# Optimization experiments

Measured on AMD Instinct MI355X. Metric: run time of the kernel, lower is better.

## Reference

```python
import jax, jax.numpy as jnp
import numpy as np

D_MODEL = 1024
N_HEADS = 16
D_HEAD = D_MODEL // N_HEADS
D_FF = 4096
EPS = 1e-5


def layernorm(x, gamma, beta):
    mu = jnp.mean(x, axis=-1, keepdims=True)
    var = jnp.var(x, axis=-1, keepdims=True)
    return (x - mu) * jax.lax.rsqrt(var + EPS) * gamma + beta


def setup_inputs() -> dict:
    key = jax.random.key(0)
    ks = jax.random.split(key, 16)
    B, T = 4, 2048
    s = 1.0 / np.sqrt(D_MODEL)
    sf = 1.0 / np.sqrt(D_FF)
    return {
        "x": jax.random.normal(ks[0], (B, T, D_MODEL), jnp.float32),
        "gate_score": jax.random.uniform(ks[1], (B,), jnp.float32),
        "Wq": jax.random.normal(ks[2], (D_MODEL, D_MODEL), jnp.float32) * s,
        "bq": jnp.zeros((D_MODEL,), jnp.float32),
        "Wk": jax.random.normal(ks[3], (D_MODEL, D_MODEL), jnp.float32) * s,
        "bk": jnp.zeros((D_MODEL,), jnp.float32),
        "Wv": jax.random.normal(ks[4], (D_MODEL, D_MODEL), jnp.float32) * s,
        "bv": jnp.zeros((D_MODEL,), jnp.float32),
        "Wo": jax.random.normal(ks[5], (D_MODEL, D_MODEL), jnp.float32) * s,
        "bo": jnp.zeros((D_MODEL,), jnp.float32),
        "W1": jax.random.normal(ks[6], (D_MODEL, D_FF), jnp.float32) * s,
        "b1": jnp.zeros((D_FF,), jnp.float32),
        "W2": jax.random.normal(ks[7], (D_FF, D_MODEL), jnp.float32) * sf,
        "b2": jnp.zeros((D_MODEL,), jnp.float32),
        "gamma1": jnp.ones((D_MODEL,), jnp.float32),
        "beta1": jnp.zeros((D_MODEL,), jnp.float32),
        "gamma2": jnp.ones((D_MODEL,), jnp.float32),
        "beta2": jnp.zeros((D_MODEL,), jnp.float32),
    }


def reference(x, gate_score, Wq, bq, Wk, bk, Wv, bv, Wo, bo,
              W1, b1, W2, b2, gamma1, beta1, gamma2, beta2):
    B, T, C = x.shape
    # --- attention sub-block (pre-norm) ---
    h = layernorm(x, gamma1, beta1)
    Q = (h @ Wq + bq).reshape(B, T, N_HEADS, D_HEAD).transpose(0, 2, 1, 3)
    K = (h @ Wk + bk).reshape(B, T, N_HEADS, D_HEAD).transpose(0, 2, 1, 3)
    V = (h @ Wv + bv).reshape(B, T, N_HEADS, D_HEAD).transpose(0, 2, 1, 3)
    scores = jnp.einsum("bhqd,bhkd->bhqk", Q, K) / np.sqrt(D_HEAD)
    causal = jnp.tril(jnp.ones((T, T), dtype=bool))  # True = keep
    scores = jnp.where(causal, scores, -jnp.inf)
    attn = jax.nn.softmax(scores, axis=-1)
    ctx = jnp.einsum("bhqk,bhkd->bhqd", attn, V)
    ctx = ctx.transpose(0, 2, 1, 3).reshape(B, T, C)
    attn_out = ctx @ Wo + bo
    x1 = x + attn_out
    # --- FFN sub-block (pre-norm) ---
    h2 = layernorm(x1, gamma2, beta2)
    ff = jax.nn.gelu(h2 @ W1 + b1, approximate=False) @ W2 + b2
    x2 = x1 + ff
    # --- gated residual ---
    g = gate_score[:, None, None]
    return x + g * (x2 - x)
```

## Files before the change

kernel.cpp:

```cpp
#include <hip/hip_runtime.h>
#include <hip/hip_bf16.h>
#include <cmath>

typedef unsigned short u16;
typedef __attribute__((ext_vector_type(8))) short short8;
typedef __attribute__((ext_vector_type(4))) float f32x4;

#define DM 1024
#define NH 16
#define DH 64
#define DFF 4096
#define BB 4
#define TT 2048
#define MROWS (BB*TT)

__device__ __forceinline__ float bu2f(u16 u) {
    union { float f; unsigned v; } c; c.v = ((unsigned)u) << 16; return c.f;
}
__device__ __forceinline__ u16 f2bu(float f) {
    __hip_bfloat16 h = __float2bfloat16(f);
    union { __hip_bfloat16 h; u16 u; } c; c.h = h; return c.u;
}
__device__ __forceinline__ void async_copy16(const u16* g, u16* l) {
    __builtin_amdgcn_global_load_lds((const __attribute__((address_space(1))) void*)g,
                                     (__attribute__((address_space(3))) void*)l, 16, 0, 0);
}

__global__ void ln_kernel(const float* __restrict__ x, const float* __restrict__ gamma,
                          const float* __restrict__ beta, u16* __restrict__ out)
{
    int row = blockIdx.x;
    int tid = threadIdx.x;
    float4 v4 = ((const float4*)(x + (size_t)row * DM))[tid];
    float v[4] = { v4.x, v4.y, v4.z, v4.w };
    float s = v[0] + v[1] + v[2] + v[3];
    float ss = v[0]*v[0] + v[1]*v[1] + v[2]*v[2] + v[3]*v[3];
    #pragma unroll
    for (int o = 32; o > 0; o >>= 1) { s += __shfl_down(s, o); ss += __shfl_down(ss, o); }
    __shared__ float red[8];
    int w = tid >> 6;
    if ((tid & 63) == 0) { red[w] = s; red[4 + w] = ss; }
    __syncthreads();
    s  = red[0] + red[1] + red[2] + red[3];
    ss = red[4] + red[5] + red[6] + red[7];
    float mu  = s * (1.0f / DM);
    float var = ss * (1.0f / DM) - mu * mu;
    float rstd = rsqrtf(var + 1e-5f);
    float4 g4 = ((const float4*)gamma)[tid];
    float4 b4 = ((const float4*)beta)[tid];
    float g[4] = { g4.x, g4.y, g4.z, g4.w };
    float b[4] = { b4.x, b4.y, b4.z, b4.w };
    ushort4 o4;
    u16* op = (u16*)&o4;
    #pragma unroll
    for (int i = 0; i < 4; i++) op[i] = f2bu((v[i] - mu) * rstd * g[i] + b[i]);
    ((ushort4*)(out + (size_t)row * DM))[tid] = o4;
}

__global__ void transpose4_f2b(const float* __restrict__ w0, const float* __restrict__ w1,
                               const float* __restrict__ w2, const float* __restrict__ w3,
                               u16* __restrict__ outQKV, u16* __restrict__ outO)
{
    __shared__ u16 tile[32][33];
    const float* in = (blockIdx.z == 0) ? w0 : (blockIdx.z == 1) ? w1
                     : (blockIdx.z == 2) ? w2 : w3;
    u16* out = (blockIdx.z < 3) ? (outQKV + (size_t)blockIdx.z * DM * DM) : outO;
    int bx = blockIdx.x * 32;
    int by = blockIdx.y * 32;
    int tx = threadIdx.x, ty = threadIdx.y;
    #pragma unroll
    for (int i = 0; i < 32; i += 8)
        tile[ty + i][tx] = f2bu(in[(size_t)(by + ty + i) * DM + bx + tx]);
    __syncthreads();
    #pragma unroll
    for (int i = 0; i < 32; i += 8)
        out[(size_t)(bx + ty + i) * DM + by + tx] = tile[tx][ty + i];
}

__global__ void transpose_f2b(const float* __restrict__ in, u16* __restrict__ out,
                              int R, int C)
{
    __shared__ u16 tile[32][33];
    int bx = blockIdx.x * 32;
    int by = blockIdx.y * 32;
    int tx = threadIdx.x, ty = threadIdx.y;
    #pragma unroll
    for (int i = 0; i < 32; i += 8)
        tile[ty + i][tx] = f2bu(in[(size_t)(by + ty + i) * C + bx + tx]);
    __syncthreads();
    #pragma unroll
    for (int i = 0; i < 32; i += 8)
        out[(size_t)(bx + ty + i) * R + by + tx] = tile[tx][ty + i];
}

#define BM 128
#define BN 128
#define BK 32

template<int EPI>
__global__ void gemm_bt(
    const u16* __restrict__ A, const u16* __restrict__ Bt,
    const float* __restrict__ bias, const float* __restrict__ bias2,
    const float* __restrict__ bias3, void* __restrict__ Cv,
    const float* __restrict__ res, const float* __restrict__ x0,
    const float* __restrict__ gate, int M, int N, int K)
{
    __shared__ __align__(16) u16 As[BM * BK];
    __shared__ __align__(16) u16 Bs[BN * BK];
    int tid = threadIdx.x;
    int lane = tid & 63, wave = tid >> 6;
    int wm = (wave & 1) * 64, wn = (wave >> 1) * 64;
    int lm = lane & 15, quad = lane >> 4;
    size_t row0 = (size_t)blockIdx.x * BM;
    size_t col0 = (size_t)blockIdx.y * BN;

    int sr = tid >> 2;
    int sk = (tid & 3) * 8;
    const u16* Ag = A  + (row0 + sr) * (size_t)K + sk;
    const u16* Bg = Bt + (col0 + sr) * (size_t)K + sk;
    u16* Asl = As + tid * 8;
    u16* Bsl = Bs + tid * 8;

    f32x4 acc[4][4];
    #pragma unroll
    for (int i = 0; i < 4; i++)
        #pragma unroll
        for (int j = 0; j < 4; j++)
            acc[i][j] = (f32x4){0.f, 0.f, 0.f, 0.f};

    for (int k0 = 0; k0 < K; k0 += BK) {
        __syncthreads();
        async_copy16(Ag + k0,                  Asl);
        async_copy16(Ag + (size_t)64 * K + k0, Asl + 64 * BK);
        async_copy16(Bg + k0,                  Bsl);
        async_copy16(Bg + (size_t)64 * K + k0, Bsl + 64 * BK);
        __syncthreads();
        short8 af[4], bfr[4];
        #pragma unroll
        for (int t = 0; t < 4; t++) {
            af[t]  = *(const short8*)&As[(wm + t * 16 + lm) * BK + quad * 8];
            bfr[t] = *(const short8*)&Bs[(wn + t * 16 + lm) * BK + quad * 8];
        }
        #pragma unroll
        for (int mt = 0; mt < 4; mt++)
            #pragma unroll
            for (int nt = 0; nt < 4; nt++)
                acc[mt][nt] = __builtin_amdgcn_mfma_f32_16x16x32_bf16(
                    af[mt], bfr[nt], acc[mt][nt], 0, 0, 0);
    }

    u16*   C16 = (u16*)Cv;
    float* Cf  = (float*)Cv;

    const float* bb = bias;
    size_t csub = 0;
    if (EPI == 0 && bias2 != nullptr) {
        size_t cbase = col0 + wn;
        if (cbase >= 2048)      { bb = bias3; csub = 2048; }
        else if (cbase >= 1024) { bb = bias2; csub = 1024; }
    }

    #pragma unroll
    for (int mt = 0; mt < 4; mt++) {
        #pragma unroll
        for (int nt = 0; nt < 4; nt++) {
            #pragma unroll
            for (int r = 0; r < 4; r++) {
                size_t row = row0 + wm + mt * 16 + quad * 4 + r;
                size_t col = col0 + wn + nt * 16 + lm;
                size_t idx = row * (size_t)N + col;
                float v = acc[mt][nt][r] + bb[col - csub];
                if (EPI == 0) {
                    C16[idx] = f2bu(v);
                } else if (EPI == 1) {
                    Cf[idx] = v + res[idx];
                } else if (EPI == 2) {
                    v = 0.5f * v * (1.0f + erff(v * 0.70710678118f));
                    C16[idx] = f2bu(v);
                } else {
                    float xv  = x0[idx];
                    float x1v = res[idx];
                    float g   = gate[row >> 11];
                    Cf[idx] = xv + g * (x1v + v - xv);
                }
            }
        }
    }
}

#define AVS 72

__global__ __launch_bounds__(256, 4) void attn_mfma(
    const u16* __restrict__ QKV, u16* __restrict__ ctx)
{
    __shared__ __align__(16) u16 Kl[64][AVS];
    __shared__ __align__(16) u16 Vt[64][AVS];
    __shared__ __align__(16) u16 Pl[4][16][AVS];

    const int LD = 3 * DM;
    int tid = threadIdx.x, lane = tid & 63, w = tid >> 6;
    int lm = lane & 15, quad = lane >> 4;

    int bi = blockIdx.x;
    int pair = bi & 15, h = (bi >> 4) & 15, b = bi >> 8;
    int t1 = 31 - pair, t2 = pair;

    const size_t hoff = (size_t)h * DH;
    const u16* Qp = QKV + (size_t)b * TT * LD + hoff;
    const u16* Kp = Qp + DM;
    const u16* Vp = Qp + 2 * DM;

    short8 aqA[2], aqB[2];
    #pragma unroll
    for (int dc = 0; dc < 2; dc++) {
        aqA[dc] = *(const short8*)(Qp + (size_t)(t1 * 64 + w * 16 + lm) * LD + dc * 32 + quad * 8);
        aqB[dc] = *(const short8*)(Qp + (size_t)(t2 * 64 + w * 16 + lm) * LD + dc * 32 + quad * 8);
    }

    int kkey = tid & 63, kdim = (tid >> 6) * 16;
    int vkey = (tid & 31) * 2, vdim = (tid >> 5) * 8;

    const u16* kb0 = Kp + (size_t)kkey * LD + kdim;
    const u16* vb0 = Vp + (size_t)vkey * LD + vdim;
    const u16* vb1 = Vp + (size_t)(vkey + 1) * LD + vdim;

    const float sc = 0.18033688011f;
    const float FM = 24.0f;
    const short s1 = (short)0x3F80;
    const short8 ones = (short8){s1, s1, s1, s1, s1, s1, s1, s1};

    uint4 kr0 = *(const uint4*)(kb0);
    uint4 kr1 = *(const uint4*)(kb0 + 8);
    uint4 vr0 = *(const uint4*)(vb0);
    uint4 vr1 = *(const uint4*)(vb1);

    #pragma unroll
    for (int ti = 0; ti < 2; ti++) {
        int tcur = (ti == 0) ? t1 : t2;
        int nch = tcur + 1;
        int q0 = tcur * 64;
        int qw = q0 + w * 16;
        short8 a0 = (ti == 0) ? aqA[0] : aqB[0];
        short8 a1 = (ti == 0) ? aqA[1] : aqB[1];
        int qv = qw + lm;

        f32x4 o[4], o5;
        #pragma unroll
        for (int ds = 0; ds < 4; ds++) o[ds] = (f32x4){0.f, 0.f, 0.f, 0.f};
        o5 = (f32x4){0.f, 0.f, 0.f, 0.f};

        for (int c = 0; c < nch; c++) {
            int kb = c * 64;
            __syncthreads();
            *(uint4*)&Kl[kkey][kdim]     = kr0;
            *(uint4*)&Kl[kkey][kdim + 8] = kr1;
            {
                const u16* p0 = (const u16*)&vr0;
                const u16* p1 = (const u16*)&vr1;
                #pragma unroll
                for (int j = 0; j < 8; j++) {
                    ushort2 pk = { p0[j], p1[j] };
                    *(ushort2*)&Vt[vdim + j][vkey] = pk;
                }
            }
            __syncthreads();

            {
                size_t offn = (c + 1 < nch) ? (size_t)(c + 1) * 64 * LD : 0;
                kr0 = *(const uint4*)(kb0 + offn);
                kr1 = *(const uint4*)(kb0 + offn + 8);
                vr0 = *(const uint4*)(vb0 + offn);
                vr1 = *(const uint4*)(vb1 + offn);
            }

            f32x4 s[4];
            #pragma unroll
            for (int ks = 0; ks < 4; ks++) s[ks] = (f32x4){0.f, 0.f, 0.f, 0.f};
            #pragma unroll
            for (int ks = 0; ks < 4; ks++) {
                short8 k0 = *(const short8*)&Kl[ks * 16 + lm][quad * 8];
                short8 k1 = *(const short8*)&Kl[ks * 16 + lm][32 + quad * 8];
                s[ks] = __builtin_amdgcn_mfma_f32_16x16x32_bf16(k0, a0, s[ks], 0, 0, 0);
                s[ks] = __builtin_amdgcn_mfma_f32_16x16x32_bf16(k1, a1, s[ks], 0, 0, 0);
            }

            bool mz = (kb + 63 > qw);
            #pragma unroll
            for (int ks = 0; ks < 4; ks++) {
                int kbase = kb + ks * 16 + quad * 4;
                ushort4 pk;
                u16* pp = (u16*)&pk;
                #pragma unroll
                for (int r = 0; r < 4; r++) {
                    float v = s[ks][r] * sc - FM;
                    if (mz && (kbase + r > qv)) v = -INFINITY;
                    pp[r] = f2bu(exp2f(v));
                }
                *(ushort4*)&Pl[w][lm][ks * 16 + quad * 4] = pk;
            }

            #pragma unroll
            for (int kc = 0; kc < 2; kc++) {
                short8 ap = *(const short8*)&Pl[w][lm][kc * 32 + quad * 8];
                #pragma unroll
                for (int ds = 0; ds < 4; ds++) {
                    short8 bv = *(const short8*)&Vt[ds * 16 + lm][kc * 32 + quad * 8];
                    o[ds] = __builtin_amdgcn_mfma_f32_16x16x32_bf16(ap, bv, o[ds], 0, 0, 0);
                }
                o5 = __builtin_amdgcn_mfma_f32_16x16x32_bf16(ap, ones, o5, 0, 0, 0);
            }
        }

        float inv[4];
        #pragma unroll
        for (int r = 0; r < 4; r++) inv[r] = 1.0f / o5[r];
        #pragma unroll
        for (int ds = 0; ds < 4; ds++)
            #pragma unroll
            for (int r = 0; r < 4; r++) {
                size_t row = (size_t)(b * TT + qw + quad * 4 + r);
                ctx[row * DM + hoff + ds * 16 + lm] = f2bu(o[ds][r] * inv[r]);
            }
    }
}

extern "C" void kernel_launch(void* const* d_in, const int* in_sizes, int n_in,
                              void* d_out, int out_size, void* d_ws, size_t ws_size,
                              hipStream_t stream)
{
    const float* x    = (const float*)d_in[0];
    const float* gate = (const float*)d_in[1];
    const float* Wq   = (const float*)d_in[2];
    const float* bq   = (const float*)d_in[3];
    const float* Wk   = (const float*)d_in[4];
    const float* bk   = (const float*)d_in[5];
    const float* Wv   = (const float*)d_in[6];
    const float* bv   = (const float*)d_in[7];
    const float* Wo   = (const float*)d_in[8];
    const float* bo   = (const float*)d_in[9];
    const float* W1   = (const float*)d_in[10];
    const float* b1   = (const float*)d_in[11];
    const float* W2   = (const float*)d_in[12];
    const float* b2   = (const float*)d_in[13];
    const float* gamma1 = (const float*)d_in[14];
    const float* beta1  = (const float*)d_in[15];
    const float* gamma2 = (const float*)d_in[16];
    const float* beta2  = (const float*)d_in[17];
    float* out = (float*)d_out;

    char* ws = (char*)d_ws;
    const size_t MB = 1024 * 1024;
    u16* WtQKV = (u16*)(ws + 0 * MB);
    u16* WtO   = (u16*)(ws + 6 * MB);
    u16* Wt1   = (u16*)(ws + 8 * MB);
    u16* Wt2   = (u16*)(ws + 16 * MB);
    u16* h     = (u16*)(ws + 24 * MB);
    u16* ctx   = (u16*)(ws + 24 * MB);
    u16* QKVb  = (u16*)(ws + 40 * MB);
    float* x1  = (float*)(ws + 40 * MB);
    u16* h2    = (u16*)(ws + 72 * MB);
    u16* ff    = (u16*)(ws + 88 * MB);

    dim3 tb(32, 8);
    transpose4_f2b<<<dim3(32, 32, 4), tb, 0, stream>>>(Wq, Wk, Wv, Wo, WtQKV, WtO);
    transpose_f2b<<<dim3(DFF / 32, DM / 32), tb, 0, stream>>>(W1, Wt1, DM, DFF);
    transpose_f2b<<<dim3(DM / 32, DFF / 32), tb, 0, stream>>>(W2, Wt2, DFF, DM);

    ln_kernel<<<MROWS, 256, 0, stream>>>(x, gamma1, beta1, h);

    gemm_bt<0><<<dim3(MROWS / BM, 3 * DM / BN), 256, 0, stream>>>(
        h, WtQKV, bq, bk, bv, QKVb, nullptr, nullptr, nullptr, MROWS, 3 * DM, DM);

    attn_mfma<<<BB * NH * 16, 256, 0, stream>>>(QKVb, ctx);

    gemm_bt<1><<<dim3(MROWS / BM, DM / BN), 256, 0, stream>>>(
        ctx, WtO, bo, nullptr, nullptr, x1, x, nullptr, nullptr, MROWS, DM, DM);

    ln_kernel<<<MROWS, 256, 0, stream>>>(x1, gamma2, beta2, h2);

    gemm_bt<2><<<dim3(MROWS / BM, DFF / BN), 256, 0, stream>>>(
        h2, Wt1, b1, nullptr, nullptr, ff, nullptr, nullptr, nullptr, MROWS, DFF, DM);

    gemm_bt<3><<<dim3(MROWS / BM, DM / BN), 256, 0, stream>>>(
        ff, Wt2, b2, nullptr, nullptr, out, x1, x, gate, MROWS, DM, DFF);
}
```

Measured before the change: 559.5 us.

## Double GEMM K-tile with XOR-swizzled LDS and split attention blocks per query tile

```diff
diff --git a/kernel.cpp b/kernel.cpp
--- a/kernel.cpp
+++ b/kernel.cpp
@@ -95,7 +95,7 @@
 
 #define BM 128
 #define BN 128
-#define BK 32
+#define BK 64
 
 template<int EPI>
 __global__ void gemm_bt(
@@ -114,12 +114,15 @@
     size_t row0 = (size_t)blockIdx.x * BM;
     size_t col0 = (size_t)blockIdx.y * BN;
 
-    int sr = tid >> 2;
-    int sk = (tid & 3) * 8;
-    const u16* Ag = A  + (row0 + sr) * (size_t)K + sk;
-    const u16* Bg = Bt + (col0 + sr) * (size_t)K + sk;
+    int sr = tid >> 3;
+    int scol = (((tid & 7) ^ (sr & 7)) * 8);
+    const u16* Ag = A  + (row0 + sr) * (size_t)K + scol;
+    const u16* Bg = Bt + (col0 + sr) * (size_t)K + scol;
     u16* Asl = As + tid * 8;
     u16* Bsl = Bs + tid * 8;
+
+    int fc0 = ((0 * 4 + quad) ^ (lm & 7)) * 8;
+    int fc1 = ((1 * 4 + quad) ^ (lm & 7)) * 8;
 
     f32x4 acc[4][4];
     #pragma unroll
@@ -131,22 +134,30 @@
     for (int k0 = 0; k0 < K; k0 += BK) {
         __syncthreads();
         async_copy16(Ag + k0,                  Asl);
+        async_copy16(Ag + (size_t)32 * K + k0, Asl + 32 * BK);
         async_copy16(Ag + (size_t)64 * K + k0, Asl + 64 * BK);
+        async_copy16(Ag + (size_t)96 * K + k0, Asl + 96 * BK);
         async_copy16(Bg + k0,                  Bsl);
+        async_copy16(Bg + (size_t)32 * K + k0, Bsl + 32 * BK);
         async_copy16(Bg + (size_t)64 * K + k0, Bsl + 64 * BK);
+        async_copy16(Bg + (size_t)96 * K + k0, Bsl + 96 * BK);
         __syncthreads();
-        short8 af[4], bfr[4];
-        #pragma unroll
-        for (int t = 0; t < 4; t++) {
-            af[t]  = *(const short8*)&As[(wm + t * 16 + lm) * BK + quad * 8];
-            bfr[t] = *(const short8*)&Bs[(wn + t * 16 + lm) * BK + quad * 8];
-        }
-        #pragma unroll
-        for (int mt = 0; mt < 4; mt++)
-            #pragma unroll
-            for (int nt = 0; nt < 4; nt++)
-                acc[mt][nt] = __builtin_amdgcn_mfma_f32_16x16x32_bf16(
-                    af[mt], bfr[nt], acc[mt][nt], 0, 0, 0);
+        #pragma unroll
+        for (int ks = 0; ks < 2; ks++) {
+            int fc = ks ? fc1 : fc0;
+            short8 af[4], bfr[4];
+            #pragma unroll
+            for (int t = 0; t < 4; t++) {
+                af[t]  = *(const short8*)&As[(wm + t * 16 + lm) * BK + fc];
+                bfr[t] = *(const short8*)&Bs[(wn + t * 16 + lm) * BK + fc];
+            }
+            #pragma unroll
+            for (int mt = 0; mt < 4; mt++)
+                #pragma unroll
+                for (int nt = 0; nt < 4; nt++)
+                    acc[mt][nt] = __builtin_amdgcn_mfma_f32_16x16x32_bf16(
+                        af[mt], bfr[nt], acc[mt][nt], 0, 0, 0);
+        }
     }
 
     u16*   C16 = (u16*)Cv;
@@ -190,7 +201,7 @@
 
 #define AVS 72
 
-__global__ __launch_bounds__(256, 4) void attn_mfma(
+__global__ __launch_bounds__(256, 5) void attn_mfma(
     const u16* __restrict__ QKV, u16* __restrict__ ctx)
 {
     __shared__ __align__(16) u16 Kl[64][AVS];
@@ -202,20 +213,21 @@
     int lm = lane & 15, quad = lane >> 4;
 
     int bi = blockIdx.x;
-    int pair = bi & 15, h = (bi >> 4) & 15, b = bi >> 8;
-    int t1 = 31 - pair, t2 = pair;
+    int tcur = 31 - (bi & 31);
+    int h = (bi >> 5) & 15, b = bi >> 9;
 
     const size_t hoff = (size_t)h * DH;
     const u16* Qp = QKV + (size_t)b * TT * LD + hoff;
     const u16* Kp = Qp + DM;
     const u16* Vp = Qp + 2 * DM;
 
-    short8 aqA[2], aqB[2];
-    #pragma unroll
-    for (int dc = 0; dc < 2; dc++) {
-        aqA[dc] = *(const short8*)(Qp + (size_t)(t1 * 64 + w * 16 + lm) * LD + dc * 32 + quad * 8);
-        aqB[dc] = *(const short8*)(Qp + (size_t)(t2 * 64 + w * 16 + lm) * LD + dc * 32 + quad * 8);
-    }
+    int nch = tcur + 1;
+    int q0 = tcur * 64;
+    int qw = q0 + w * 16;
+    int qv = qw + lm;
+
+    short8 a0 = *(const short8*)(Qp + (size_t)(qw + lm) * LD + quad * 8);
+    short8 a1 = *(const short8*)(Qp + (size_t)(qw + lm) * LD + 32 + quad * 8);
 
     int kkey = tid & 63, kdim = (tid >> 6) * 16;
     int vkey = (tid & 31) * 2, vdim = (tid >> 5) * 8;
@@ -234,94 +246,83 @@
     uint4 vr0 = *(const uint4*)(vb0);
     uint4 vr1 = *(const uint4*)(vb1);
 
-    #pragma unroll
-    for (int ti = 0; ti < 2; ti++) {
-        int tcur = (ti == 0) ? t1 : t2;
-        int nch = tcur + 1;
-        int q0 = tcur * 64;
-        int qw = q0 + w * 16;
-        short8 a0 = (ti == 0) ? aqA[0] : aqB[0];
-        short8 a1 = (ti == 0) ? aqA[1] : aqB[1];
-        int qv = qw + lm;
-
-        f32x4 o[4], o5;
-        #pragma unroll
-        for (int ds = 0; ds < 4; ds++) o[ds] = (f32x4){0.f, 0.f, 0.f, 0.f};
-        o5 = (f32x4){0.f, 0.f, 0.f, 0.f};
-
-        for (int c = 0; c < nch; c++) {
-            int kb = c * 64;
-            __syncthreads();
-            *(uint4*)&Kl[kkey][kdim]     = kr0;
-            *(uint4*)&Kl[kkey][kdim + 8] = kr1;
-            {
-                const u16* p0 = (const u16*)&vr0;
-                const u16* p1 = (const u16*)&vr1;
-                #pragma unroll
-                for (int j = 0; j < 8; j++) {
-                    ushort2 pk = { p0[j], p1[j] };
-                    *(ushort2*)&Vt[vdim + j][vkey] = pk;
-                }
-            }
-            __syncthreads();
-
-            {
-                size_t offn = (c + 1 < nch) ? (size_t)(c + 1) * 64 * LD : 0;
-                kr0 = *(const uint4*)(kb0 + offn);
-                kr1 = *(const uint4*)(kb0 + offn + 8);
-                vr0 = *(const uint4*)(vb0 + offn);
-                vr1 = *(const uint4*)(vb1 + offn);
-            }
-
-            f32x4 s[4];
-            #pragma unroll
-            for (int ks = 0; ks < 4; ks++) s[ks] = (f32x4){0.f, 0.f, 0.f, 0.f};
-            #pragma unroll
-            for (int ks = 0; ks < 4; ks++) {
-                short8 k0 = *(const short8*)&Kl[ks * 16 + lm][quad * 8];
-                short8 k1 = *(const short8*)&Kl[ks * 16 + lm][32 + quad * 8];
-                s[ks] = __builtin_amdgcn_mfma_f32_16x16x32_bf16(k0, a0, s[ks], 0, 0, 0);
-                s[ks] = __builtin_amdgcn_mfma_f32_16x16x32_bf16(k1, a1, s[ks], 0, 0, 0);
-            }
-
-            bool mz = (kb + 63 > qw);
-            #pragma unroll
-            for (int ks = 0; ks < 4; ks++) {
-                int kbase = kb + ks * 16 + quad * 4;
-                ushort4 pk;
-                u16* pp = (u16*)&pk;
-                #pragma unroll
-                for (int r = 0; r < 4; r++) {
-                    float v = s[ks][r] * sc - FM;
-                    if (mz && (kbase + r > qv)) v = -INFINITY;
-                    pp[r] = f2bu(exp2f(v));
-                }
-                *(ushort4*)&Pl[w][lm][ks * 16 + quad * 4] = pk;
-            }
-
-            #pragma unroll
-            for (int kc = 0; kc < 2; kc++) {
-                short8 ap = *(const short8*)&Pl[w][lm][kc * 32 + quad * 8];
-                #pragma unroll
-                for (int ds = 0; ds < 4; ds++) {
-                    short8 bv = *(const short8*)&Vt[ds * 16 + lm][kc * 32 + quad * 8];
-                    o[ds] = __builtin_amdgcn_mfma_f32_16x16x32_bf16(ap, bv, o[ds], 0, 0, 0);
-                }
-                o5 = __builtin_amdgcn_mfma_f32_16x16x32_bf16(ap, ones, o5, 0, 0, 0);
-            }
-        }
-
-        float inv[4];
-        #pragma unroll
-        for (int r = 0; r < 4; r++) inv[r] = 1.0f / o5[r];
-        #pragma unroll
-        for (int ds = 0; ds < 4; ds++)
+    f32x4 o[4], o5;
+    #pragma unroll
+    for (int ds = 0; ds < 4; ds++) o[ds] = (f32x4){0.f, 0.f, 0.f, 0.f};
+    o5 = (f32x4){0.f, 0.f, 0.f, 0.f};
+
+    for (int c = 0; c < nch; c++) {
+        int kb = c * 64;
+        __syncthreads();
+        *(uint4*)&Kl[kkey][kdim]     = kr0;
+        *(uint4*)&Kl[kkey][kdim + 8] = kr1;
+        {
+            const u16* p0 = (const u16*)&vr0;
+            const u16* p1 = (const u16*)&vr1;
+            #pragma unroll
+            for (int j = 0; j < 8; j++) {
+                ushort2 pk = { p0[j], p1[j] };
+                *(ushort2*)&Vt[vdim + j][vkey] = pk;
+            }
+        }
+        __syncthreads();
+
+        {
+            size_t offn = (c + 1 < nch) ? (size_t)(c + 1) * 64 * LD : 0;
+            kr0 = *(const uint4*)(kb0 + offn);
+            kr1 = *(const uint4*)(kb0 + offn + 8);
+            vr0 = *(const uint4*)(vb0 + offn);
+            vr1 = *(const uint4*)(vb1 + offn);
+        }
+
+        f32x4 s[4];
+        #pragma unroll
+        for (int ks = 0; ks < 4; ks++) s[ks] = (f32x4){0.f, 0.f, 0.f, 0.f};
+        #pragma unroll
+        for (int ks = 0; ks < 4; ks++) {
+            short8 k0 = *(const short8*)&Kl[ks * 16 + lm][quad * 8];
+            short8 k1 = *(const short8*)&Kl[ks * 16 + lm][32 + quad * 8];
+            s[ks] = __builtin_amdgcn_mfma_f32_16x16x32_bf16(k0, a0, s[ks], 0, 0, 0);
+            s[ks] = __builtin_amdgcn_mfma_f32_16x16x32_bf16(k1, a1, s[ks], 0, 0, 0);
+        }
+
+        bool mz = (kb + 63 > qw);
+        #pragma unroll
+        for (int ks = 0; ks < 4; ks++) {
+            int kbase = kb + ks * 16 + quad * 4;
+            ushort4 pk;
+            u16* pp = (u16*)&pk;
             #pragma unroll
             for (int r = 0; r < 4; r++) {
-                size_t row = (size_t)(b * TT + qw + quad * 4 + r);
-                ctx[row * DM + hoff + ds * 16 + lm] = f2bu(o[ds][r] * inv[r]);
-            }
+                float v = s[ks][r] * sc - FM;
+                if (mz && (kbase + r > qv)) v = -INFINITY;
+                pp[r] = f2bu(exp2f(v));
+            }
+            *(ushort4*)&Pl[w][lm][ks * 16 + quad * 4] = pk;
+        }
+
+        #pragma unroll
+        for (int kc = 0; kc < 2; kc++) {
+            short8 ap = *(const short8*)&Pl[w][lm][kc * 32 + quad * 8];
+            #pragma unroll
+            for (int ds = 0; ds < 4; ds++) {
+                short8 bv = *(const short8*)&Vt[ds * 16 + lm][kc * 32 + quad * 8];
+                o[ds] = __builtin_amdgcn_mfma_f32_16x16x32_bf16(ap, bv, o[ds], 0, 0, 0);
+            }
+            o5 = __builtin_amdgcn_mfma_f32_16x16x32_bf16(ap, ones, o5, 0, 0, 0);
+        }
     }
+
+    float inv[4];
+    #pragma unroll
+    for (int r = 0; r < 4; r++) inv[r] = 1.0f / o5[r];
+    #pragma unroll
+    for (int ds = 0; ds < 4; ds++)
+        #pragma unroll
+        for (int r = 0; r < 4; r++) {
+            size_t row = (size_t)(b * TT + qw + quad * 4 + r);
+            ctx[row * DM + hoff + ds * 16 + lm] = f2bu(o[ds][r] * inv[r]);
+        }
 }
 
 extern "C" void kernel_launch(void* const* d_in, const int* in_sizes, int n_in,
@@ -371,7 +372,7 @@
     gemm_bt<0><<<dim3(MROWS / BM, 3 * DM / BN), 256, 0, stream>>>(
         h, WtQKV, bq, bk, bv, QKVb, nullptr, nullptr, nullptr, MROWS, 3 * DM, DM);
 
-    attn_mfma<<<BB * NH * 16, 256, 0, stream>>>(QKVb, ctx);
+    attn_mfma<<<BB * NH * 32, 256, 0, stream>>>(QKVb, ctx);
 
     gemm_bt<1><<<dim3(MROWS / BM, DM / BN), 256, 0, stream>>>(
         ctx, WtO, bo, nullptr, nullptr, x1, x, nullptr, nullptr, MROWS, DM, DM);
```

Result: slower. 594.9 us (+6.3%).
